# Optimization experiments

Hardware: AMD Instinct MI355X
Metric: run time of the kernel (lower is better)

The kernel has to match this reference:

```python
import jax, jax.numpy as jnp
import numpy as np

HID, E, S, L_CAP, EPS = 768, 1536, 128, 512, 1e-5


def _rope_seq(x):
    """RoPE along axis 1. x: [b, n, 2, s]."""
    n, s = x.shape[1], x.shape[-1]
    half = s // 2
    inv_freq = jnp.power(10000.0, -jnp.arange(half, dtype=x.dtype) / half)  # [half]
    sinusoid = jnp.arange(n, dtype=x.dtype)[:, None, None] * inv_freq       # [n,1,half]
    sin, cos = jnp.sin(sinusoid), jnp.cos(sinusoid)
    x1, x2 = jnp.split(x, 2, axis=-1)
    return jnp.concatenate([x1 * cos - x2 * sin, x2 * cos + x1 * sin], axis=-1)


def setup_inputs() -> dict:
    key = jax.random.key(0)
    ks = jax.random.split(key, 6)
    B, L = 32, 512
    return {
        "x": jax.random.normal(ks[0], (B, L, HID), dtype=jnp.float32),
        "ln_gamma": jnp.ones((HID,), jnp.float32),
        "ln_beta": jnp.zeros((HID,), jnp.float32),
        "uv_W": jax.random.normal(ks[1], (HID, 2 * E + S), jnp.float32) * 0.02,
        "uv_b": jnp.zeros((2 * E + S,), jnp.float32),
        "gamma_qk": jax.random.normal(ks[2], (2, S), jnp.float32) * 0.02,
        "beta_qk": jnp.zeros((2, S), jnp.float32),
        "w_rel": jax.random.normal(ks[3], (2 * L_CAP - 1,), jnp.float32) * 0.02,
        "o_W": jax.random.normal(ks[4], (E, HID), jnp.float32) * 0.02,
        "o_b": jnp.zeros((HID,), jnp.float32),
    }


def reference(x, ln_gamma, ln_beta, uv_W, uv_b, gamma_qk, beta_qk, w_rel, o_W, o_b):
    L = x.shape[1]
    shortcut = x
    # LayerNorm
    mu = jnp.mean(x, axis=-1, keepdims=True)
    var = jnp.mean(jnp.square(x - mu), axis=-1, keepdims=True)
    xn = (x - mu) * jax.lax.rsqrt(var + EPS) * ln_gamma + ln_beta
    # uv projection + silu, split into u, v, base
    uv = jax.nn.silu(xn @ uv_W + uv_b)                       # [b, n, 2e+s]
    u, v, base = jnp.split(uv, [E, 2 * E], axis=-1)          # [b,n,e], [b,n,e], [b,n,s]
    # per-head affine then RoPE -> q, k
    base = base[..., None, :] * gamma_qk + beta_qk           # [b, n, 2, s]
    base = _rope_seq(base)
    q, k = base[..., 0, :], base[..., 1, :]
    # relu^2 attention kernel with Toeplitz relative position bias
    qk = jnp.einsum('bnd,bmd->bnm', q, k)
    idx = jnp.arange(L)
    bias = w_rel[idx[None, :] - idx[:, None] + L - 1]        # bias[i,j] = w[j-i+L-1]
    kernel = jnp.square(jax.nn.relu(qk / L + bias))
    # gated value aggregation + output projection + residual
    out = u * jnp.einsum('bnm,bme->bne', kernel, v)
    out = out @ o_W + o_b
    return out + shortcut
```

## Files before the change

### kernel.cpp

```cpp
#include <hip/hip_runtime.h>
#include <hip/hip_bf16.h>
#include <math.h>

typedef __bf16 bf16x8 __attribute__((ext_vector_type(8)));
typedef float f32x4 __attribute__((ext_vector_type(4)));
typedef unsigned short u16x4 __attribute__((ext_vector_type(4)));

#define AS1P const __attribute__((address_space(1))) void*
#define AS3P __attribute__((address_space(3))) void*

__device__ __forceinline__ float b2f(unsigned short h) {
    unsigned int u = ((unsigned int)h) << 16;
    return __builtin_bit_cast(float, u);
}
__device__ __forceinline__ unsigned short f2b(float f) {
    unsigned int u = __builtin_bit_cast(unsigned int, f);
    u += 0x7FFFu + ((u >> 16) & 1u);
    return (unsigned short)(u >> 16);
}
__device__ __forceinline__ float silu(float c) {
    return c * __builtin_amdgcn_rcpf(1.0f + __expf(-c));
}

__global__ __launch_bounds__(256) void k_pre(const float* __restrict__ uv_W,
                                             unsigned short* __restrict__ uvWT,
                                             const float* __restrict__ o_W,
                                             unsigned short* __restrict__ oWT,
                                             const float* __restrict__ x,
                                             const float* __restrict__ g,
                                             const float* __restrict__ bia,
                                             unsigned short* __restrict__ xn) {
    __shared__ float tile[32][33];
    __shared__ float ss[4], sq[4];
    int b = blockIdx.x;
    int t = threadIdx.x;
    if (b < 3552) {
        const float* src;
        unsigned short* dst;
        int R, C, bx, by;
        if (b < 2400) {
            src = uv_W; dst = uvWT; R = 768; C = 3200;
            bx = b % 100; by = b / 100;
        } else {
            int b2 = b - 2400;
            src = o_W; dst = oWT; R = 1536; C = 768;
            bx = b2 % 24; by = b2 / 24;
        }
        int tx = t & 31, ty = t >> 5;
        int r0 = by << 5, c0 = bx << 5;
#pragma unroll
        for (int i = 0; i < 4; ++i)
            tile[ty + 8 * i][tx] = src[(long long)(r0 + ty + 8 * i) * C + c0 + tx];
        __syncthreads();
#pragma unroll
        for (int i = 0; i < 4; ++i)
            dst[(long long)(c0 + ty + 8 * i) * R + r0 + tx] = f2b(tile[tx][ty + 8 * i]);
        return;
    }
    int row = b - 3552;
    const float* xr = x + (long long)row * 768;
    float v0 = xr[t], v1 = xr[t + 256], v2 = xr[t + 512];
    float s = v0 + v1 + v2;
    float q = v0 * v0 + v1 * v1 + v2 * v2;
#pragma unroll
    for (int off = 32; off > 0; off >>= 1) {
        s += __shfl_xor(s, off);
        q += __shfl_xor(q, off);
    }
    int w = t >> 6;
    if ((t & 63) == 0) { ss[w] = s; sq[w] = q; }
    __syncthreads();
    float S_ = ss[0] + ss[1] + ss[2] + ss[3];
    float Q_ = sq[0] + sq[1] + sq[2] + sq[3];
    float mu = S_ * (1.0f / 768.0f);
    float var = Q_ * (1.0f / 768.0f) - mu * mu;
    float rs = rsqrtf(var + 1e-5f);
    unsigned short* xo = xn + (long long)row * 768;
    xo[t]       = f2b((v0 - mu) * rs * g[t]       + bia[t]);
    xo[t + 256] = f2b((v1 - mu) * rs * g[t + 256] + bia[t + 256]);
    xo[t + 512] = f2b((v2 - mu) * rs * g[t + 512] + bia[t + 512]);
}

__global__ __launch_bounds__(256) void k_bs(const unsigned short* __restrict__ A,
                                            const unsigned short* __restrict__ B,
                                            const float* __restrict__ bias,
                                            const float* __restrict__ gqk,
                                            const float* __restrict__ bqk,
                                            unsigned short* __restrict__ q,
                                            unsigned short* __restrict__ k) {
    __shared__ __align__(16) unsigned short sh[12288];
    unsigned short* As_ = sh;
    unsigned short* Bs_ = sh + 4096;
    int t = threadIdx.x;
    int w = t >> 6, lane = t & 63;
    int wr = w >> 1, wc = w & 1;
    int by = blockIdx.x;
    const unsigned short* Ab = A + (long long)by * 64 * 768;

    f32x4 acc[2][4];
#pragma unroll
    for (int m = 0; m < 2; ++m)
#pragma unroll
        for (int n = 0; n < 4; ++n) acc[m][n] = (f32x4){0.f, 0.f, 0.f, 0.f};

    int rowA = (w << 3) + (lane >> 3);
    int colA = (lane & 7) << 3;

    for (int k0 = 0; k0 < 768; k0 += 64) {
#pragma unroll
        for (int i = 0; i < 2; ++i) {
            int r = (i << 5) + rowA;
            __builtin_amdgcn_global_load_lds(
                (AS1P)(Ab + (long long)r * 768 + k0 + colA),
                (AS3P)(&As_[(i << 11) + (w << 9)]), 16, 0, 0);
        }
#pragma unroll
        for (int i = 0; i < 4; ++i) {
            int r = (i << 5) + rowA;
            __builtin_amdgcn_global_load_lds(
                (AS1P)(B + (long long)r * 768 + k0 + colA),
                (AS3P)(&Bs_[(i << 11) + (w << 9)]), 16, 0, 0);
        }
        __syncthreads();
#pragma unroll
        for (int ks = 0; ks < 2; ++ks) {
            bf16x8 af[2], bfr[4];
#pragma unroll
            for (int m = 0; m < 2; ++m)
                af[m] = *(const bf16x8*)&As_[((wr << 5) + (m << 4) + (lane & 15)) * 64 +
                                             (ks << 5) + ((lane >> 4) << 3)];
#pragma unroll
            for (int n = 0; n < 4; ++n)
                bfr[n] = *(const bf16x8*)&Bs_[((wc << 6) + (n << 4) + (lane & 15)) * 64 +
                                              (ks << 5) + ((lane >> 4) << 3)];
#pragma unroll
            for (int m = 0; m < 2; ++m)
#pragma unroll
                for (int n = 0; n < 4; ++n)
                    acc[m][n] = __builtin_amdgcn_mfma_f32_16x16x32_bf16(bfr[n], af[m],
                                                                        acc[m][n], 0, 0, 0);
        }
        __syncthreads();
    }

    unsigned short* tile = sh;
    int c15 = lane & 15, qq = lane >> 4;
    int lrowb = (wr << 5) + c15;
    int colb = (wc << 6) + (qq << 2);
#pragma unroll
    for (int m = 0; m < 2; ++m) {
#pragma unroll
        for (int n = 0; n < 4; ++n) {
            int lrow = lrowb + (m << 4);
            int gcol = colb + (n << 4);
            f32x4 a = acc[m][n];
            u16x4 o;
#pragma unroll
            for (int i = 0; i < 4; ++i)
                o[i] = f2b(silu(a[i] + bias[gcol + i]));
            *(u16x4*)(tile + lrow * 128 + gcol) = o;
        }
    }
    __syncthreads();

    int s = t & 127, rgrp = t >> 7;
    int pr = s ^ 64;
    float gq0 = gqk[s], bq0 = bqk[s];
    float gqp = gqk[pr], bqp = bqk[pr];
    float gk0 = gqk[128 + s], bk0 = bqk[128 + s];
    float gkp = gqk[128 + pr], bkp = bqk[128 + pr];
    float invf = __expf((float)(s & 63) * -0.14391156831f);
    float sign = (s < 64) ? -1.0f : 1.0f;
#pragma unroll 4
    for (int rr = 0; rr < 32; ++rr) {
        int lrow = rgrp * 32 + rr;
        int grow = (by << 6) + lrow;
        int l = grow & 511;
        float th = (float)l * invf;
        float sn, cs;
        __sincosf(th, &sn, &cs);
        float b0 = b2f(tile[lrow * 128 + s]);
        float bp = b2f(tile[lrow * 128 + pr]);
        q[(long long)grow * 128 + s] = f2b((b0 * gq0 + bq0) * cs + sign * (bp * gqp + bqp) * sn);
        k[(long long)grow * 128 + s] = f2b((b0 * gk0 + bk0) * cs + sign * (bp * gkp + bkp) * sn);
    }
}

__device__ __forceinline__ bf16x8 ldsread(const unsigned short* p) {
    bf16x8 r;
    unsigned int off =
        (unsigned int)(unsigned long long)(__attribute__((address_space(3))) const void*)p;
    asm volatile("ds_read_b128 %0, %1" : "=v"(r) : "v"(off));
    return r;
}
__device__ __forceinline__ void stage_half(const unsigned short* __restrict__ g, int ldk,
                                           unsigned short* lds, int t) {
#pragma unroll
    for (int i = 0; i < 2; ++i) {
        int slot = t + (i << 9);
        int row = slot >> 2;
        int gs = (slot & 3) ^ ((slot >> 3) & 3);
        __builtin_amdgcn_global_load_lds(
            (AS1P)(g + (long long)row * ldk + (gs << 3)),
            (AS3P)(lds + slot * 8), 16, 0, 0);
    }
}

template <bool SWAP, int NT, int NF>
__device__ __forceinline__ void kloop8(const unsigned short* __restrict__ Ab,
                                       const unsigned short* __restrict__ Bb,
                                       unsigned short* As, unsigned short* Bs,
                                       f32x4 (&acc)[8][NF], int tid,
                                       int wr, int wc, int c15, int qq, int gq) {
    constexpr int K = NT * 64;
    stage_half(Ab, K, As + 0, tid);
    stage_half(Bb, K, Bs + 0, tid);
    stage_half(Ab + 32, K, As + 8192, tid);
    stage_half(Bb + 32, K, Bs + 8192, tid);
    stage_half(Ab + 64, K, As + 16384, tid);
    stage_half(Bb + 64, K, Bs + 16384, tid);
    asm volatile("s_waitcnt vmcnt(8)" ::: "memory");
    __builtin_amdgcn_s_barrier();

    bf16x8 bfr[NF], af[4];
    for (int t = 0; t < NT; ++t) {
        const int b = t & 1;
        const unsigned short* A0 = As + b * 16384;
        const unsigned short* B0 = Bs + b * 16384;
#pragma unroll
        for (int p = 0; p < 4; ++p) {
            const int ks = p >> 1, mh = p & 1;
            const unsigned short* At = A0 + ks * 8192;
            const unsigned short* Bt = B0 + ks * 8192;
            if (mh == 0) {
#pragma unroll
                for (int n = 0; n < NF; ++n)
                    bfr[n] = ldsread(Bt + (wc * (NF * 16) + n * 16 + c15) * 32 + gq * 8);
            }
#pragma unroll
            for (int j = 0; j < 4; ++j)
                af[j] = ldsread(At + (wr * 128 + (mh * 4 + j) * 16 + c15) * 32 + gq * 8);
            if (p == 0) {
                if (t + 1 < NT)
                    stage_half(Ab + (t + 1) * 64 + 32, K,
                               As + (((t + 1) & 1) * 2 + 1) * 8192, tid);
            } else if (p == 1) {
                if (t + 1 < NT)
                    stage_half(Bb + (t + 1) * 64 + 32, K,
                               Bs + (((t + 1) & 1) * 2 + 1) * 8192, tid);
            } else if (p == 2) {
                if (t + 2 < NT)
                    stage_half(Ab + (t + 2) * 64, K, As + (b * 2) * 8192, tid);
            } else {
                if (t + 2 < NT)
                    stage_half(Bb + (t + 2) * 64, K, Bs + (b * 2) * 8192, tid);
            }
            __builtin_amdgcn_s_barrier();
            asm volatile("s_waitcnt lgkmcnt(0)" ::: "memory");
            __builtin_amdgcn_sched_barrier(0);
            __builtin_amdgcn_s_setprio(1);
#pragma unroll
            for (int j = 0; j < 4; ++j)
#pragma unroll
                for (int n = 0; n < NF; ++n) {
                    if constexpr (SWAP)
                        acc[mh * 4 + j][n] = __builtin_amdgcn_mfma_f32_16x16x32_bf16(
                            bfr[n], af[j], acc[mh * 4 + j][n], 0, 0, 0);
                    else
                        acc[mh * 4 + j][n] = __builtin_amdgcn_mfma_f32_16x16x32_bf16(
                            af[j], bfr[n], acc[mh * 4 + j][n], 0, 0, 0);
                }
            __builtin_amdgcn_s_setprio(0);
            if (p == 1) {
                if (t < NT - 1)
                    asm volatile("s_waitcnt vmcnt(8)" ::: "memory");
                else
                    asm volatile("s_waitcnt vmcnt(0)" ::: "memory");
            } else if (p == 3) {
                if (t < NT - 2)
                    asm volatile("s_waitcnt vmcnt(8)" ::: "memory");
                else if (t == NT - 2)
                    asm volatile("s_waitcnt vmcnt(4)" ::: "memory");
            }
            __builtin_amdgcn_sched_barrier(0);
            __builtin_amdgcn_s_barrier();
        }
    }
}

template <int EPI, int SWZ, int NT, int NF>
__global__ __launch_bounds__(512, 2) void k8(const unsigned short* __restrict__ A,
                                             const unsigned short* __restrict__ B,
                                             long long strideA, long long strideB,
                                             void* p0, void* p1, void* p2,
                                             const void* p3) {
    constexpr int K = NT * 64;
    __shared__ __align__(16) unsigned short As[2][2][256 * 32];
    __shared__ __align__(16) unsigned short Bs[2][2][256 * 32];
    int tid = threadIdx.x;
    int w = tid >> 6, lane = tid & 63;
    int wr = w >> 2, wc = w & 3;
    int c15 = lane & 15, qq = lane >> 4;
    int gq = qq ^ ((c15 >> 1) & 3);
    int bx = blockIdx.x, by = blockIdx.y, bz = blockIdx.z;
    if constexpr (SWZ == 1) {
        int gx = gridDim.x;
        int nb = gx * gridDim.y;
        int bid = by * gx + bx;
        int s = (bid & 7) * (nb >> 3) + (bid >> 3);
        bx = s % gx;
        by = s / gx;
    } else if constexpr (SWZ == 2) {
        int gx = gridDim.x, gy = gridDim.y;
        int nb = gx * gy * gridDim.z;
        int bid = (bz * gy + by) * gx + bx;
        int s = (bid & 7) * (nb >> 3) + (bid >> 3);
        bx = s % gx;
        by = (s / gx) % gy;
        bz = s / (gx * gy);
    }
    const unsigned short* Ab = A + bz * strideA + (long long)by * 256 * K;
    const unsigned short* Bb = B + bz * strideB + (long long)bx * (NF * 64) * K;

    f32x4 acc[8][NF];
#pragma unroll
    for (int m = 0; m < 8; ++m)
#pragma unroll
        for (int n = 0; n < NF; ++n) acc[m][n] = (f32x4){0.f, 0.f, 0.f, 0.f};

    bool swapped = true;
    if constexpr (EPI == 10) {
        swapped = (bx < 6);
        if (swapped)
            kloop8<true, NT, NF>(Ab, Bb, &As[0][0][0], &Bs[0][0][0], acc, tid, wr, wc, c15, qq, gq);
        else
            kloop8<false, NT, NF>(Ab, Bb, &As[0][0][0], &Bs[0][0][0], acc, tid, wr, wc, c15, qq, gq);
    } else {
        kloop8<true, NT, NF>(Ab, Bb, &As[0][0][0], &Bs[0][0][0], acc, tid, wr, wc, c15, qq, gq);
    }

    if constexpr (EPI == 10) {
        if (swapped) {
            int rowb = by * 256 + wr * 128 + c15;
            int colb = bx * 256 + wc * 64 + (qq << 2);
#pragma unroll
            for (int m = 0; m < 8; ++m) {
#pragma unroll
                for (int n = 0; n < NF; ++n) {
                    int R = rowb + m * 16;
                    int C = colb + n * 16;
                    f32x4 a = acc[m][n];
                    f32x4 bb = *(const f32x4*)((const float*)p3 + C);
                    u16x4 o;
#pragma unroll
                    for (int i = 0; i < 4; ++i) o[i] = f2b(silu(a[i] + bb[i]));
                    *(u16x4*)((unsigned short*)p0 + (long long)R * 1536 + C) = o;
                }
            }
        } else {
            int rowb = by * 256 + wr * 128 + (qq << 2);
            int colb = bx * 256 + wc * 64 + c15;
#pragma unroll
            for (int m = 0; m < 8; ++m) {
#pragma unroll
                for (int n = 0; n < NF; ++n) {
                    int R = rowb + m * 16;
                    int C = colb + n * 16;
                    float bias = ((const float*)p3)[C];
                    f32x4 a = acc[m][n];
                    u16x4 o;
#pragma unroll
                    for (int i = 0; i < 4; ++i) o[i] = f2b(silu(a[i] + bias));
                    int bb2 = R >> 9, mm = R & 511;
                    *(u16x4*)((unsigned short*)p1 +
                              ((long long)bb2 * 1600 + (C - 1536)) * 512 + mm) = o;
                }
            }
        }
    } else if constexpr (EPI == 1) {
        const float* wrel = (const float*)p1;
        int rowb = by * 256 + wr * 128 + c15;
        int colb = bx * (NF * 64) + wc * (NF * 16) + (qq << 2);
#pragma unroll
        for (int m = 0; m < 8; ++m) {
#pragma unroll
            for (int n = 0; n < NF; ++n) {
                int R = rowb + m * 16;
                int C = colb + n * 16;
                f32x4 a = acc[m][n];
                int base = C - R + 511;
                u16x4 o;
#pragma unroll
                for (int i = 0; i < 4; ++i) {
                    float val = a[i] * (1.0f / 512.0f) + wrel[base + i];
                    val = fmaxf(val, 0.0f);
                    o[i] = f2b(val * val);
                }
                *(u16x4*)((unsigned short*)p0 + ((long long)(bz * 512 + R)) * 512 + C) = o;
            }
        }
    } else if constexpr (EPI == 2) {
        int rowb = by * 256 + wr * 128 + c15;
        int colb = bx * (NF * 64) + wc * (NF * 16) + (qq << 2);
#pragma unroll
        for (int m = 0; m < 8; ++m) {
#pragma unroll
            for (int n = 0; n < NF; ++n) {
                int R = rowb + m * 16;
                int C = colb + n * 16;
                f32x4 a = acc[m][n];
                long long idx = ((long long)(bz * 512 + R)) * 1536 + C;
                u16x4 uu = *(const u16x4*)((const unsigned short*)p1 + idx);
                u16x4 o;
#pragma unroll
                for (int i = 0; i < 4; ++i) o[i] = f2b(a[i] * b2f(uu[i]));
                *(u16x4*)((unsigned short*)p0 + idx) = o;
            }
        }
    } else {
        int rowb = by * 256 + wr * 128 + c15;
        int colb = bx * (NF * 64) + wc * (NF * 16) + (qq << 2);
#pragma unroll
        for (int m = 0; m < 8; ++m) {
#pragma unroll
            for (int n = 0; n < NF; ++n) {
                int R = rowb + m * 16;
                int C = colb + n * 16;
                f32x4 a = acc[m][n];
                long long idx = (long long)R * 768 + C;
                f32x4 xv = *(const f32x4*)((const float*)p2 + idx);
                f32x4 ob = *(const f32x4*)((const float*)p1 + C);
                f32x4 o;
#pragma unroll
                for (int i = 0; i < 4; ++i) o[i] = a[i] + ob[i] + xv[i];
                *(f32x4*)((float*)p0 + idx) = o;
            }
        }
    }
}

extern "C" void kernel_launch(void* const* d_in, const int* in_sizes, int n_in,
                              void* d_out, int out_size, void* d_ws, size_t ws_size,
                              hipStream_t stream) {
    const float* x     = (const float*)d_in[0];
    const float* ln_g  = (const float*)d_in[1];
    const float* ln_b  = (const float*)d_in[2];
    const float* uv_W  = (const float*)d_in[3];
    const float* uv_b  = (const float*)d_in[4];
    const float* g_qk  = (const float*)d_in[5];
    const float* b_qk  = (const float*)d_in[6];
    const float* w_rel = (const float*)d_in[7];
    const float* o_W   = (const float*)d_in[8];
    const float* o_b   = (const float*)d_in[9];
    float* out = (float*)d_out;

    char* ws = (char*)d_ws;
    size_t off = 0;
    auto alloc = [&](size_t bytes) {
        void* p = ws + off;
        off += (bytes + 255) & ~(size_t)255;
        return p;
    };
    unsigned short* uvWT = (unsigned short*)alloc(3200ll * 768 * 2);
    unsigned short* oWT  = (unsigned short*)alloc(832ll * 1536 * 2);
    unsigned short* xn   = (unsigned short*)alloc(16384ll * 768 * 2);
    unsigned short* u    = (unsigned short*)alloc(16384ll * 1536 * 2);
    unsigned short* vT   = (unsigned short*)alloc(32ll * 1600 * 512 * 2);
    unsigned short* q    = (unsigned short*)alloc(32ll * 512 * 128 * 2);
    unsigned short* k    = (unsigned short*)alloc((32ll * 512 + 128) * 128 * 2);
    unsigned short* P     = xn;
    unsigned short* gated = u;

    k_pre<<<19936, 256, 0, stream>>>(uv_W, uvWT, o_W, oWT, x, ln_g, ln_b, xn);
    k8<10, 1, 12, 4><<<dim3(12, 64), 512, 0, stream>>>(
        xn, uvWT, 0, 0, (void*)u, (void*)vT, nullptr, (const void*)uv_b);
    k_bs<<<256, 256, 0, stream>>>(xn, uvWT + 3072ll * 768, uv_b + 3072,
                                  g_qk, b_qk, q, k);
    k8<1, 2, 2, 2><<<dim3(4, 2, 32), 512, 0, stream>>>(
        q, k, 512ll * 128, 512ll * 128, (void*)P, (void*)w_rel, nullptr, nullptr);
    k8<2, 2, 8, 3><<<dim3(8, 2, 32), 512, 0, stream>>>(
        P, vT, 512ll * 512, 1600ll * 512, (void*)gated, (void*)u, nullptr, nullptr);
    k8<3, 1, 24, 3><<<dim3(4, 64), 512, 0, stream>>>(
        gated, oWT, 0, 0, (void*)out, (void*)o_b, (void*)x, nullptr);
}
```

Baseline: 260.2 us.

## Make GEMM kernels persistent and prefetch next tile before epilogue

Converts the k8 GEMM kernels to a 1D grid of 256 blocks, each processing TPB tiles in sequence with the tile swizzle computed at compile time. Before running the epilogue for the current tile, each block issues the global-to-LDS prologue loads for its next tile, so epilogue stores overlap with the next tile's loads. This reduces wave-quantization tail effects for the uv and PV GEMMs. The trade-off is added loop and control complexity, and a risk of LDS reuse hazards while the next tile's prefetch is in flight.

Measured after the change: 262.4 us. Within noise of the previous version (+0.8%).

```diff
diff --git a/kernel.cpp b/kernel.cpp
--- a/kernel.cpp
+++ b/kernel.cpp
@@ -206,19 +206,25 @@
     }
 }
 
-template <bool SWAP, int NT, int NF>
-__device__ __forceinline__ void kloop8(const unsigned short* __restrict__ Ab,
-                                       const unsigned short* __restrict__ Bb,
-                                       unsigned short* As, unsigned short* Bs,
-                                       f32x4 (&acc)[8][NF], int tid,
-                                       int wr, int wc, int c15, int qq, int gq) {
-    constexpr int K = NT * 64;
+template <int K>
+__device__ __forceinline__ void prologue8(const unsigned short* __restrict__ Ab,
+                                          const unsigned short* __restrict__ Bb,
+                                          unsigned short* As, unsigned short* Bs, int tid) {
     stage_half(Ab, K, As + 0, tid);
     stage_half(Bb, K, Bs + 0, tid);
     stage_half(Ab + 32, K, As + 8192, tid);
     stage_half(Bb + 32, K, Bs + 8192, tid);
     stage_half(Ab + 64, K, As + 16384, tid);
     stage_half(Bb + 64, K, Bs + 16384, tid);
+}
+
+template <bool SWAP, int NT, int NF>
+__device__ __forceinline__ void body8(const unsigned short* __restrict__ Ab,
+                                      const unsigned short* __restrict__ Bb,
+                                      unsigned short* As, unsigned short* Bs,
+                                      f32x4 (&acc)[8][NF], int tid,
+                                      int wr, int wc, int c15, int gq) {
+    constexpr int K = NT * 64;
     asm volatile("s_waitcnt vmcnt(8)" ::: "memory");
     __builtin_amdgcn_s_barrier();
 
@@ -288,13 +294,15 @@
     }
 }
 
-template <int EPI, int SWZ, int NT, int NF>
+template <int EPI, int TX, int TY, int TZ, int TPB, int NT, int NF>
 __global__ __launch_bounds__(512, 2) void k8(const unsigned short* __restrict__ A,
                                              const unsigned short* __restrict__ B,
                                              long long strideA, long long strideB,
                                              void* p0, void* p1, void* p2,
                                              const void* p3) {
     constexpr int K = NT * 64;
+    constexpr int NTILES = TX * TY * TZ;
+    constexpr int NBLK = NTILES / TPB;
     __shared__ __align__(16) unsigned short As[2][2][256 * 32];
     __shared__ __align__(16) unsigned short Bs[2][2][256 * 32];
     int tid = threadIdx.x;
@@ -302,47 +310,87 @@
     int wr = w >> 2, wc = w & 3;
     int c15 = lane & 15, qq = lane >> 4;
     int gq = qq ^ ((c15 >> 1) & 3);
-    int bx = blockIdx.x, by = blockIdx.y, bz = blockIdx.z;
-    if constexpr (SWZ == 1) {
-        int gx = gridDim.x;
-        int nb = gx * gridDim.y;
-        int bid = by * gx + bx;
-        int s = (bid & 7) * (nb >> 3) + (bid >> 3);
-        bx = s % gx;
-        by = s / gx;
-    } else if constexpr (SWZ == 2) {
-        int gx = gridDim.x, gy = gridDim.y;
-        int nb = gx * gy * gridDim.z;
-        int bid = (bz * gy + by) * gx + bx;
-        int s = (bid & 7) * (nb >> 3) + (bid >> 3);
-        bx = s % gx;
-        by = (s / gx) % gy;
-        bz = s / (gx * gy);
-    }
+    int pid = blockIdx.x;
+
+    int bx, by, bz;
+    auto decomp = [&](int f) {
+        int s = (f & 7) * (NTILES >> 3) + (f >> 3);
+        bx = s % TX;
+        by = (s / TX) % TY;
+        bz = s / (TX * TY);
+    };
+    decomp(pid);
     const unsigned short* Ab = A + bz * strideA + (long long)by * 256 * K;
     const unsigned short* Bb = B + bz * strideB + (long long)bx * (NF * 64) * K;
-
-    f32x4 acc[8][NF];
-#pragma unroll
-    for (int m = 0; m < 8; ++m)
-#pragma unroll
-        for (int n = 0; n < NF; ++n) acc[m][n] = (f32x4){0.f, 0.f, 0.f, 0.f};
-
-    bool swapped = true;
-    if constexpr (EPI == 10) {
-        swapped = (bx < 6);
-        if (swapped)
-            kloop8<true, NT, NF>(Ab, Bb, &As[0][0][0], &Bs[0][0][0], acc, tid, wr, wc, c15, qq, gq);
-        else
-            kloop8<false, NT, NF>(Ab, Bb, &As[0][0][0], &Bs[0][0][0], acc, tid, wr, wc, c15, qq, gq);
-    } else {
-        kloop8<true, NT, NF>(Ab, Bb, &As[0][0][0], &Bs[0][0][0], acc, tid, wr, wc, c15, qq, gq);
-    }
-
-    if constexpr (EPI == 10) {
-        if (swapped) {
-            int rowb = by * 256 + wr * 128 + c15;
-            int colb = bx * 256 + wc * 64 + (qq << 2);
+    prologue8<K>(Ab, Bb, &As[0][0][0], &Bs[0][0][0], tid);
+
+    for (int j = 0; j < TPB; ++j) {
+        f32x4 acc[8][NF];
+#pragma unroll
+        for (int m = 0; m < 8; ++m)
+#pragma unroll
+            for (int n = 0; n < NF; ++n) acc[m][n] = (f32x4){0.f, 0.f, 0.f, 0.f};
+
+        bool swapped = true;
+        if constexpr (EPI == 10) {
+            swapped = (bx < 6);
+            if (swapped)
+                body8<true, NT, NF>(Ab, Bb, &As[0][0][0], &Bs[0][0][0], acc, tid, wr, wc, c15, gq);
+            else
+                body8<false, NT, NF>(Ab, Bb, &As[0][0][0], &Bs[0][0][0], acc, tid, wr, wc, c15, gq);
+        } else {
+            body8<true, NT, NF>(Ab, Bb, &As[0][0][0], &Bs[0][0][0], acc, tid, wr, wc, c15, gq);
+        }
+        int ebx = bx, eby = by, ebz = bz;
+        if (j + 1 < TPB) {
+            decomp(pid + (j + 1) * NBLK);
+            Ab = A + bz * strideA + (long long)by * 256 * K;
+            Bb = B + bz * strideB + (long long)bx * (NF * 64) * K;
+            prologue8<K>(Ab, Bb, &As[0][0][0], &Bs[0][0][0], tid);
+        }
+
+        if constexpr (EPI == 10) {
+            if (swapped) {
+                int rowb = eby * 256 + wr * 128 + c15;
+                int colb = ebx * 256 + wc * 64 + (qq << 2);
+#pragma unroll
+                for (int m = 0; m < 8; ++m) {
+#pragma unroll
+                    for (int n = 0; n < NF; ++n) {
+                        int R = rowb + m * 16;
+                        int C = colb + n * 16;
+                        f32x4 a = acc[m][n];
+                        f32x4 bb = *(const f32x4*)((const float*)p3 + C);
+                        u16x4 o;
+#pragma unroll
+                        for (int i = 0; i < 4; ++i) o[i] = f2b(silu(a[i] + bb[i]));
+                        *(u16x4*)((unsigned short*)p0 + (long long)R * 1536 + C) = o;
+                    }
+                }
+            } else {
+                int rowb = eby * 256 + wr * 128 + (qq << 2);
+                int colb = ebx * 256 + wc * 64 + c15;
+#pragma unroll
+                for (int m = 0; m < 8; ++m) {
+#pragma unroll
+                    for (int n = 0; n < NF; ++n) {
+                        int R = rowb + m * 16;
+                        int C = colb + n * 16;
+                        float bias = ((const float*)p3)[C];
+                        f32x4 a = acc[m][n];
+                        u16x4 o;
+#pragma unroll
+                        for (int i = 0; i < 4; ++i) o[i] = f2b(silu(a[i] + bias));
+                        int bb2 = R >> 9, mm = R & 511;
+                        *(u16x4*)((unsigned short*)p1 +
+                                  ((long long)bb2 * 1600 + (C - 1536)) * 512 + mm) = o;
+                    }
+                }
+            }
+        } else if constexpr (EPI == 1) {
+            const float* wrel = (const float*)p1;
+            int rowb = eby * 256 + wr * 128 + c15;
+            int colb = ebx * (NF * 64) + wc * (NF * 16) + (qq << 2);
 #pragma unroll
             for (int m = 0; m < 8; ++m) {
 #pragma unroll
@@ -350,90 +398,54 @@
                     int R = rowb + m * 16;
                     int C = colb + n * 16;
                     f32x4 a = acc[m][n];
-                    f32x4 bb = *(const f32x4*)((const float*)p3 + C);
+                    int base = C - R + 511;
                     u16x4 o;
 #pragma unroll
-                    for (int i = 0; i < 4; ++i) o[i] = f2b(silu(a[i] + bb[i]));
-                    *(u16x4*)((unsigned short*)p0 + (long long)R * 1536 + C) = o;
-                }
-            }
-        } else {
-            int rowb = by * 256 + wr * 128 + (qq << 2);
-            int colb = bx * 256 + wc * 64 + c15;
+                    for (int i = 0; i < 4; ++i) {
+                        float val = a[i] * (1.0f / 512.0f) + wrel[base + i];
+                        val = fmaxf(val, 0.0f);
+                        o[i] = f2b(val * val);
+                    }
+                    *(u16x4*)((unsigned short*)p0 +
+                              ((long long)(ebz * 512 + R)) * 512 + C) = o;
+                }
+            }
+        } else if constexpr (EPI == 2) {
+            int rowb = eby * 256 + wr * 128 + c15;
+            int colb = ebx * (NF * 64) + wc * (NF * 16) + (qq << 2);
 #pragma unroll
             for (int m = 0; m < 8; ++m) {
 #pragma unroll
                 for (int n = 0; n < NF; ++n) {
                     int R = rowb + m * 16;
                     int C = colb + n * 16;
-                    float bias = ((const float*)p3)[C];
                     f32x4 a = acc[m][n];
+                    long long idx = ((long long)(ebz * 512 + R)) * 1536 + C;
+                    u16x4 uu = *(const u16x4*)((const unsigned short*)p1 + idx);
                     u16x4 o;
 #pragma unroll
-                    for (int i = 0; i < 4; ++i) o[i] = f2b(silu(a[i] + bias));
-                    int bb2 = R >> 9, mm = R & 511;
-                    *(u16x4*)((unsigned short*)p1 +
-                              ((long long)bb2 * 1600 + (C - 1536)) * 512 + mm) = o;
-                }
-            }
-        }
-    } else if constexpr (EPI == 1) {
-        const float* wrel = (const float*)p1;
-        int rowb = by * 256 + wr * 128 + c15;
-        int colb = bx * (NF * 64) + wc * (NF * 16) + (qq << 2);
-#pragma unroll
-        for (int m = 0; m < 8; ++m) {
-#pragma unroll
-            for (int n = 0; n < NF; ++n) {
-                int R = rowb + m * 16;
-                int C = colb + n * 16;
-                f32x4 a = acc[m][n];
-                int base = C - R + 511;
-                u16x4 o;
-#pragma unroll
-                for (int i = 0; i < 4; ++i) {
-                    float val = a[i] * (1.0f / 512.0f) + wrel[base + i];
-                    val = fmaxf(val, 0.0f);
-                    o[i] = f2b(val * val);
-                }
-                *(u16x4*)((unsigned short*)p0 + ((long long)(bz * 512 + R)) * 512 + C) = o;
-            }
-        }
-    } else if constexpr (EPI == 2) {
-        int rowb = by * 256 + wr * 128 + c15;
-        int colb = bx * (NF * 64) + wc * (NF * 16) + (qq << 2);
-#pragma unroll
-        for (int m = 0; m < 8; ++m) {
-#pragma unroll
-            for (int n = 0; n < NF; ++n) {
-                int R = rowb + m * 16;
-                int C = colb + n * 16;
-                f32x4 a = acc[m][n];
-                long long idx = ((long long)(bz * 512 + R)) * 1536 + C;
-                u16x4 uu = *(const u16x4*)((const unsigned short*)p1 + idx);
-                u16x4 o;
-#pragma unroll
-                for (int i = 0; i < 4; ++i) o[i] = f2b(a[i] * b2f(uu[i]));
-                *(u16x4*)((unsigned short*)p0 + idx) = o;
-            }
-        }
-    } else {
-        int rowb = by * 256 + wr * 128 + c15;
-        int colb = bx * (NF * 64) + wc * (NF * 16) + (qq << 2);
-#pragma unroll
-        for (int m = 0; m < 8; ++m) {
-#pragma unroll
-            for (int n = 0; n < NF; ++n) {
-                int R = rowb + m * 16;
-                int C = colb + n * 16;
-                f32x4 a = acc[m][n];
-                long long idx = (long long)R * 768 + C;
-                f32x4 xv = *(const f32x4*)((const float*)p2 + idx);
-                f32x4 ob = *(const f32x4*)((const float*)p1 + C);
-                f32x4 o;
-#pragma unroll
-                for (int i = 0; i < 4; ++i) o[i] = a[i] + ob[i] + xv[i];
-                *(f32x4*)((float*)p0 + idx) = o;
+                    for (int i = 0; i < 4; ++i) o[i] = f2b(a[i] * b2f(uu[i]));
+                    *(u16x4*)((unsigned short*)p0 + idx) = o;
+                }
+            }
+        } else {
+            int rowb = eby * 256 + wr * 128 + c15;
+            int colb = ebx * (NF * 64) + wc * (NF * 16) + (qq << 2);
+#pragma unroll
+            for (int m = 0; m < 8; ++m) {
+#pragma unroll
+                for (int n = 0; n < NF; ++n) {
+                    int R = rowb + m * 16;
+                    int C = colb + n * 16;
+                    f32x4 a = acc[m][n];
+                    long long idx = (long long)R * 768 + C;
+                    f32x4 xv = *(const f32x4*)((const float*)p2 + idx);
+                    f32x4 ob = *(const f32x4*)((const float*)p1 + C);
+                    f32x4 o;
+#pragma unroll
+                    for (int i = 0; i < 4; ++i) o[i] = a[i] + ob[i] + xv[i];
+                    *(f32x4*)((float*)p0 + idx) = o;
+                }
             }
         }
     }
@@ -472,14 +484,14 @@
     unsigned short* gated = u;
 
     k_pre<<<19936, 256, 0, stream>>>(uv_W, uvWT, o_W, oWT, x, ln_g, ln_b, xn);
-    k8<10, 1, 12, 4><<<dim3(12, 64), 512, 0, stream>>>(
+    k8<10, 12, 64, 1, 3, 12, 4><<<256, 512, 0, stream>>>(
         xn, uvWT, 0, 0, (void*)u, (void*)vT, nullptr, (const void*)uv_b);
     k_bs<<<256, 256, 0, stream>>>(xn, uvWT + 3072ll * 768, uv_b + 3072,
                                   g_qk, b_qk, q, k);
-    k8<1, 2, 2, 2><<<dim3(4, 2, 32), 512, 0, stream>>>(
+    k8<1, 4, 2, 32, 1, 2, 2><<<256, 512, 0, stream>>>(
         q, k, 512ll * 128, 512ll * 128, (void*)P, (void*)w_rel, nullptr, nullptr);
-    k8<2, 2, 8, 3><<<dim3(8, 2, 32), 512, 0, stream>>>(
+    k8<2, 8, 2, 32, 2, 8, 3><<<256, 512, 0, stream>>>(
         P, vT, 512ll * 512, 1600ll * 512, (void*)gated, (void*)u, nullptr, nullptr);
-    k8<3, 1, 24, 3><<<dim3(4, 64), 512, 0, stream>>>(
+    k8<3, 4, 64, 1, 1, 24, 3><<<256, 512, 0, stream>>>(
         gated, oWT, 0, 0, (void*)out, (void*)o_b, (void*)x, nullptr);
 }
```
